# Kernel optimization log

Hardware: AMD Instinct MI355X
Metric: run time of the kernel (lower is better)

The kernel has to match this reference:

```python
import jax, jax.numpy as jnp
import numpy as np

QSIGN = jnp.array([1.0, -1.0, -1.0, -1.0], dtype=jnp.float32)
IDENT = jnp.array([1.0, 0.0, 0.0, 0.0], dtype=jnp.float32)


def quat_multiply(a, b):
    aw, ax, ay, az = a[..., 0], a[..., 1], a[..., 2], a[..., 3]
    bw, bx, by, bz = b[..., 0], b[..., 1], b[..., 2], b[..., 3]
    return jnp.stack([
        aw * bw - ax * bx - ay * by - az * bz,
        aw * bx + ax * bw + ay * bz - az * by,
        aw * by - ax * bz + ay * bw + az * bx,
        aw * bz + ax * by - ay * bx + az * bw], axis=-1)


def quat_to_rot(q):
    w, x, y, z = q[..., 0], q[..., 1], q[..., 2], q[..., 3]
    r = jnp.stack([
        w * w + x * x - y * y - z * z, 2 * (x * y - w * z), 2 * (x * z + w * y),
        2 * (x * y + w * z), w * w - x * x + y * y - z * z, 2 * (y * z - w * x),
        2 * (x * z - w * y), 2 * (y * z + w * x), w * w - x * x - y * y + z * z], axis=-1)
    return r.reshape(q.shape[:-1] + (3, 3))


def quat_rotate(q, v):
    return jnp.einsum('...ij,...j->...i', quat_to_rot(q), v)


def mlp(z, W1, b1, W2, b2):
    return jax.nn.relu(z @ W1 + b1) @ W2 + b2


def setup_inputs() -> dict:
    key = jax.random.key(0)
    ks = jax.random.split(key, 24)
    B, N, H, E, M, O, T = 2, 512, 64, 32, 64, 64, 64
    x = jax.random.normal(ks[0], (B, N, 3), dtype=jnp.float32)
    q = jax.random.normal(ks[1], (B, N, 4), dtype=jnp.float32)
    q = q / jnp.linalg.norm(q, axis=-1, keepdims=True)  # unit quats
    h = jax.random.normal(ks[2], (B, N, H), dtype=jnp.float32)
    e = jax.random.normal(ks[3], (B, N, N, E), dtype=jnp.float32)
    node_mask = jnp.ones((B, N), dtype=bool)

    def lin(k, fi, fo):
        return jax.random.normal(k, (fi, fo), dtype=jnp.float32) / np.sqrt(fi)

    msg_in = 2 * H + E + 9  # 169
    inp = dict(x=x, quats=q, h=h, e=e, node_mask=node_mask,
               Wm1=lin(ks[4], msg_in, T), bm1=jnp.zeros((T,)),
               Wm2=lin(ks[5], T, M), bm2=jnp.zeros((M,)),
               Wf1=lin(ks[6], H + M, T), bf1=jnp.zeros((T,)),
               Wf2=lin(ks[7], T, O), bf2=jnp.zeros((O,)),
               Wt1=lin(ks[8], M, T), bt1=jnp.zeros((T,)),
               Wt2=lin(ks[9], T, 3), bt2=jnp.zeros((3,)),
               Wq1=lin(ks[10], M, T), bq1=jnp.zeros((T,)),
               Wq2=lin(ks[11], T, 4), bq2=jnp.zeros((4,)))
    return inp


def reference(x, quats, h, e, node_mask,
              Wm1, bm1, Wm2, bm2, Wf1, bf1, Wf2, bf2,
              Wt1, bt1, Wt2, bt2, Wq1, bq1, Wq2, bq2):
    B, N, H = h.shape
    eye = jnp.eye(N, dtype=bool)[None]
    msg_mask = node_mask[:, :, None] & node_mask[:, None, :] & ~eye  # [B,N,N]
    n_nodes = node_mask.sum(axis=-1).astype(x.dtype)  # [B]

    # inverse frame of node j: rot = conj(q_j)/|q_j|^2, applied as R_j^-1 (x_i - t_j)
    q_inv = (quats * QSIGN) / jnp.sum(quats * quats, axis=-1, keepdims=True)

    diff = x[:, :, None, :] - x[:, None, :, :]            # [B,N,N,3], x_i - x_j
    d2 = jnp.sum(diff * diff, axis=-1)                    # [B,N,N]
    qdot = jnp.abs(jnp.einsum('bik,bjk->bij', quats, quats))
    local_x = quat_rotate(q_inv[:, None, :, :], diff)     # R_j^-1 (x_i - x_j)
    local_q = quat_multiply(q_inv[:, None, :, :], quats[:, :, None, :])  # q_j^-1 * q_i

    hi = jnp.broadcast_to(h[:, :, None, :], (B, N, N, H))
    hj = jnp.broadcast_to(h[:, None, :, :], (B, N, N, H))
    feat = jnp.concatenate([hi, hj, e, local_x, local_q,
                            d2[..., None], qdot[..., None]], axis=-1)

    m = mlp(feat, Wm1, bm1, Wm2, bm2) * msg_mask[..., None]  # [B,N,N,M]
    msum = m.sum(axis=-2)                                    # [B,N,M]

    o = mlp(jnp.concatenate([h, msum], axis=-1), Wf1, bf1, Wf2, bf2)

    dx = mlp(m, Wt1, bt1, Wt2, bt2) * msg_mask[..., None]    # [B,N,N,3]

    dq = mlp(msum, Wq1, bq1, Wq2, bq2)                       # [B,N,4]
    dq = jnp.where(node_mask[..., None], dq, IDENT)
    dq = dq / jnp.maximum(jnp.linalg.norm(dq, axis=-1, keepdims=True), 1e-12)

    upd_q = quat_multiply(quats, dq)
    upd_q = jnp.where(node_mask[..., None], upd_q, IDENT)
    upd_q = upd_q / jnp.linalg.norm(upd_q, axis=-1, keepdims=True)  # normalize_quats=True

    # rotate dx[i,j] by updated frame of node j, aggregate over j
    rot_dx = quat_rotate(upd_q[:, None, :, :], dx).sum(axis=-2)     # [B,N,3]
    upd_x = x + rot_dx / (n_nodes[:, None, None] - 1.0)
    return upd_q, upd_x, o
```

## Files before the change

### kernel.cpp

```cpp
#include <hip/hip_runtime.h>
#include <math.h>
#include <stdint.h>

#define B_ 2
#define N_ 512

#define WS_WBF   0
#define WS_NGEO  7680
#define WS_APRE  15872
#define WS_BPREF 81408
#define WS_MPART 146944
#define WS_DXBUF 278016

typedef short short8v __attribute__((ext_vector_type(8)));
typedef float f32x4 __attribute__((ext_vector_type(4)));

union FragU { int4 i; short8v s; };
union PackU { uint32_t w[4]; short8v s; };

static __device__ inline uint32_t pk2(float lo, float hi) {
    uint32_t r;
    asm volatile("v_cvt_pk_bf16_f32 %0, %1, %2" : "=v"(r) : "v"(lo), "v"(hi));
    return r;
}
static __device__ inline short f2bs(float f) {
    uint32_t u = __float_as_uint(f);
    u = (u + 0x7FFFu + ((u >> 16) & 1u)) >> 16;
    return (short)u;
}

__global__ void k_prep(const float* __restrict__ Wm1, const float* __restrict__ Wm2,
                       const float* __restrict__ Wt1, const float* __restrict__ Wt2,
                       short* __restrict__ wbf)
{
    const int id = blockIdx.x * 256 + threadIdx.x;
    if (id < 4608) {
        const int ch = id / 72, p = id % 72;
        float v1 = 0.f, v2 = 0.f, v3 = 0.f;
        if (p < 64) {
            if (p < 32) v1 = Wm1[(128 + p) * 64 + ch];
            else if (p < 41) v1 = Wm1[(160 + p - 32) * 64 + ch];
            const int s = p >> 5, ee = p & 7, gg = (p >> 3) & 3;
            const int k1 = 32 * s + 16 * (ee >> 2) + 4 * gg + (ee & 3);
            v2 = Wm2[k1 * 64 + ch];
            v3 = Wt1[k1 * 64 + ch];
        }
        wbf[id] = f2bs(v1);
        wbf[4608 + id] = f2bs(v2);
        wbf[9216 + id] = f2bs(v3);
    } else if (id < 5760) {
        const int idx = id - 4608;
        const int d = idx / 72, p = idx % 72;
        float v = 0.f;
        if (p < 64 && d < 3) {
            const int s = p >> 5, ee = p & 7, gg = (p >> 3) & 3;
            const int k1 = 32 * s + 16 * (ee >> 2) + 4 * gg + (ee & 3);
            v = Wt2[k1 * 3 + d];
        }
        wbf[13824 + idx] = f2bs(v);
    }
}

__global__ __launch_bounds__(256) void k_node_pre(
    const float* __restrict__ x,
    const float* __restrict__ quats,
    const float* __restrict__ h,
    const float* __restrict__ Wm1,
    const float* __restrict__ bm1,
    float* __restrict__ ngeo,
    float* __restrict__ Apre,
    float* __restrict__ BpreF)
{
    __shared__ float sW[128 * 64];
    __shared__ float sh[4][64];

    const int tid = threadIdx.x;
    for (int idx = tid; idx < 128 * 64 / 4; idx += 256)
        ((float4*)sW)[idx] = ((const float4*)Wm1)[idx];

    const int wv = tid >> 6;
    const int c = tid & 63;
    const int node = blockIdx.x * 4 + wv;

    sh[wv][c] = h[node * 64 + c];
    __syncthreads();

    float a = bm1[c];
    float bv = 0.f;
#pragma unroll 8
    for (int k = 0; k < 64; ++k) {
        const float hk = sh[wv][k];
        a  = fmaf(hk, sW[k * 64 + c], a);
        bv = fmaf(hk, sW[(64 + k) * 64 + c], bv);
    }
    Apre[node * 64 + c] = a;
    const int aa = c >> 4, gg = (c >> 2) & 3, bb = c & 3;
    BpreF[(node >> 4) * 1024 + ((node & 15) + 16 * gg) * 16 + 4 * aa + bb] = bv;

    if (c == 0) {
        ngeo[node * 8 + 0] = x[node * 3 + 0];
        ngeo[node * 8 + 1] = x[node * 3 + 1];
        ngeo[node * 8 + 2] = x[node * 3 + 2];
        ngeo[node * 8 + 3] = 0.f;
        ngeo[node * 8 + 4] = quats[node * 4 + 0];
        ngeo[node * 8 + 5] = quats[node * 4 + 1];
        ngeo[node * 8 + 6] = quats[node * 4 + 2];
        ngeo[node * 8 + 7] = quats[node * 4 + 3];
    }
}

__global__ __launch_bounds__(512, 2) void k_edge(
    const float* __restrict__ e,
    const float* __restrict__ ngeo,
    const float* __restrict__ Apre,
    const float* __restrict__ BpreF,
    const short* __restrict__ wbf,
    const float* __restrict__ bm2,
    const float* __restrict__ bt1,
    const float* __restrict__ bt2,
    float* __restrict__ mpart, float* __restrict__ dxbuf)
{
    __shared__ __align__(16) short Ws[14976];
    __shared__ float msLDS[4][64];

    const int tid = threadIdx.x;

    for (int idx = tid; idx < 1872; idx += 512)
        ((int4*)Ws)[idx] = ((const int4*)wbf)[idx];
    __syncthreads();

    const short* W1s = Ws;
    const short* W2s = Ws + 4608;
    const short* W3s = Ws + 9216;
    const short* W4s = Ws + 13824;

    const int w = tid >> 6;
    const int l = tid & 63;
    const int g = l >> 4;
    const int c = l & 15;

    const int ig = blockIdx.x >> 1;
    const int half = blockIdx.x & 1;
    const int ni = ig * 4 + (w >> 1);
    const int b = ni >> 9;
    const int i = ni & 511;
    const int quarter = half * 2 + (w & 1);
    const int j0w = quarter * 128;

    const float4 gi0 = ((const float4*)ngeo)[ni * 2 + 0];
    const float4 gi1 = ((const float4*)ngeo)[ni * 2 + 1];
    const float xi0 = gi0.x, xi1 = gi0.y, xi2 = gi0.z;
    const float qi0 = gi1.x, qi1 = gi1.y, qi2 = gi1.z, qi3 = gi1.w;

    float apre[16], bm2r[16], bt1r[16], bt2r[4];
#pragma unroll
    for (int q = 0; q < 16; ++q) {
        const int row = 16 * (q >> 2) + 4 * g + (q & 3);
        apre[q] = Apre[ni * 64 + row];
        bm2r[q] = bm2[row];
        bt1r[q] = bt1[row];
    }
#pragma unroll
    for (int q = 0; q < 4; ++q) {
        const int d = 4 * g + q;
        bt2r[q] = (d < 3) ? bt2[d] : 0.f;
    }

    float msum[16];
#pragma unroll
    for (int q = 0; q < 16; ++q) msum[q] = 0.f;

#pragma unroll 2
    for (int t = 0; t < 8; ++t) {
        const int j0m = j0w + t * 16;
        const int nj = b * N_ + j0m + c;

        const float* ep = e + ((size_t)(b * N_ + i) * N_ + j0m + c) * 32 + g * 8;
        const float4 e0 = *(const float4*)ep;
        const float4 e1 = *(const float4*)(ep + 4);
        const float4 n0 = ((const float4*)ngeo)[nj * 2 + 0];
        const float4 n1 = ((const float4*)ngeo)[nj * 2 + 1];
        const float* bp = BpreF + (size_t)(nj >> 4) * 1024 + l * 16;
        const float4 bi0 = ((const float4*)bp)[0];
        const float4 bi1 = ((const float4*)bp)[1];
        const float4 bi2 = ((const float4*)bp)[2];
        const float4 bi3 = ((const float4*)bp)[3];

        const float xj0 = n0.x, xj1 = n0.y, xj2 = n0.z;
        const float qj0 = n1.x, qj1 = n1.y, qj2 = n1.z, qj3 = n1.w;
        const float dsum = qj0 * qj0 + qj1 * qj1 + qj2 * qj2 + qj3 * qj3;
        const float inv = __builtin_amdgcn_rcpf(dsum);
        const float qw = qj0 * inv, qx = -qj1 * inv;
        const float qy = -qj2 * inv, qz = -qj3 * inv;
        const float d0 = xi0 - xj0, d1 = xi1 - xj1, d2v = xi2 - xj2;
        const float dd = d0 * d0 + d1 * d1 + d2v * d2v;
        const float qd = fabsf(qi0 * qj0 + qi1 * qj1 + qi2 * qj2 + qi3 * qj3);
        const float ww = qw * qw, xx = qx * qx, yy = qy * qy, zz = qz * qz;
        const float xy = qx * qy, xz = qx * qz, yz = qy * qz;
        const float wx = qw * qx, wy = qw * qy, wz = qw * qz;
        const float lx0 = (ww + xx - yy - zz) * d0 + 2.f * (xy - wz) * d1 + 2.f * (xz + wy) * d2v;
        const float lx1 = 2.f * (xy + wz) * d0 + (ww - xx + yy - zz) * d1 + 2.f * (yz - wx) * d2v;
        const float lx2 = 2.f * (xz - wy) * d0 + 2.f * (yz + wx) * d1 + (ww - xx - yy + zz) * d2v;
        const float lq0 = qw * qi0 - qx * qi1 - qy * qi2 - qz * qi3;
        const float lq1 = qw * qi1 + qx * qi0 + qy * qi3 - qz * qi2;
        const float lq2 = qw * qi2 - qx * qi3 + qy * qi0 + qz * qi1;
        const float lq3 = qw * qi3 + qx * qi2 - qy * qi1 + qz * qi0;

        PackU y0, yg;
        y0.w[0] = pk2(e0.x, e0.y); y0.w[1] = pk2(e0.z, e0.w);
        y0.w[2] = pk2(e1.x, e1.y); y0.w[3] = pk2(e1.z, e1.w);
        const uint32_t w0 = pk2(lx0, lx1), w1 = pk2(lx2, lq0);
        const uint32_t w2 = pk2(lq1, lq2), w3 = pk2(lq3, dd);
        const uint32_t wq = pk2(qd, 0.f);
        yg.w[0] = (g == 0) ? w0 : ((g == 1) ? wq : 0u);
        yg.w[1] = (g == 0) ? w1 : 0u;
        yg.w[2] = (g == 0) ? w2 : 0u;
        yg.w[3] = (g == 0) ? w3 : 0u;

        f32x4 acc1[4];
        acc1[0][0] = apre[0] + bi0.x;  acc1[0][1] = apre[1] + bi0.y;
        acc1[0][2] = apre[2] + bi0.z;  acc1[0][3] = apre[3] + bi0.w;
        acc1[1][0] = apre[4] + bi1.x;  acc1[1][1] = apre[5] + bi1.y;
        acc1[1][2] = apre[6] + bi1.z;  acc1[1][3] = apre[7] + bi1.w;
        acc1[2][0] = apre[8] + bi2.x;  acc1[2][1] = apre[9] + bi2.y;
        acc1[2][2] = apre[10] + bi2.z; acc1[2][3] = apre[11] + bi2.w;
        acc1[3][0] = apre[12] + bi3.x; acc1[3][1] = apre[13] + bi3.y;
        acc1[3][2] = apre[14] + bi3.z; acc1[3][3] = apre[15] + bi3.w;
#pragma unroll
        for (int nt = 0; nt < 4; ++nt) {
            FragU xw0, xw1;
            xw0.i = *(const int4*)&W1s[(16 * nt + c) * 72 + g * 8];
            xw1.i = *(const int4*)&W1s[(16 * nt + c) * 72 + 32 + g * 8];
            acc1[nt] = __builtin_amdgcn_mfma_f32_16x16x32_bf16(xw0.s, y0.s, acc1[nt], 0, 0, 0);
            acc1[nt] = __builtin_amdgcn_mfma_f32_16x16x32_bf16(xw1.s, yg.s, acc1[nt], 0, 0, 0);
        }

        PackU by1[2];
#pragma unroll
        for (int s = 0; s < 2; ++s) {
            const f32x4 a0 = acc1[2 * s], a1 = acc1[2 * s + 1];
            by1[s].w[0] = pk2(fmaxf(a0[0], 0.f), fmaxf(a0[1], 0.f));
            by1[s].w[1] = pk2(fmaxf(a0[2], 0.f), fmaxf(a0[3], 0.f));
            by1[s].w[2] = pk2(fmaxf(a1[0], 0.f), fmaxf(a1[1], 0.f));
            by1[s].w[3] = pk2(fmaxf(a1[2], 0.f), fmaxf(a1[3], 0.f));
        }

        f32x4 acc2[4];
#pragma unroll
        for (int nt = 0; nt < 4; ++nt) {
            acc2[nt][0] = bm2r[nt * 4 + 0]; acc2[nt][1] = bm2r[nt * 4 + 1];
            acc2[nt][2] = bm2r[nt * 4 + 2]; acc2[nt][3] = bm2r[nt * 4 + 3];
        }
#pragma unroll
        for (int nt = 0; nt < 4; ++nt)
#pragma unroll
            for (int s = 0; s < 2; ++s) {
                FragU xw;
                xw.i = *(const int4*)&W2s[(16 * nt + c) * 72 + s * 32 + g * 8];
                acc2[nt] = __builtin_amdgcn_mfma_f32_16x16x32_bf16(
                    xw.s, by1[s].s, acc2[nt], 0, 0, 0);
            }

        const float maskf = (j0m + c == i) ? 0.f : 1.f;
#pragma unroll
        for (int nt = 0; nt < 4; ++nt) {
            acc2[nt][0] *= maskf; acc2[nt][1] *= maskf;
            acc2[nt][2] *= maskf; acc2[nt][3] *= maskf;
            msum[nt * 4 + 0] += acc2[nt][0];
            msum[nt * 4 + 1] += acc2[nt][1];
            msum[nt * 4 + 2] += acc2[nt][2];
            msum[nt * 4 + 3] += acc2[nt][3];
        }

        PackU by2[2];
#pragma unroll
        for (int s = 0; s < 2; ++s) {
            const f32x4 a0 = acc2[2 * s], a1 = acc2[2 * s + 1];
            by2[s].w[0] = pk2(a0[0], a0[1]);
            by2[s].w[1] = pk2(a0[2], a0[3]);
            by2[s].w[2] = pk2(a1[0], a1[1]);
            by2[s].w[3] = pk2(a1[2], a1[3]);
        }

        f32x4 acc3[4];
#pragma unroll
        for (int nt = 0; nt < 4; ++nt) {
            acc3[nt][0] = bt1r[nt * 4 + 0]; acc3[nt][1] = bt1r[nt * 4 + 1];
            acc3[nt][2] = bt1r[nt * 4 + 2]; acc3[nt][3] = bt1r[nt * 4 + 3];
        }
#pragma unroll
        for (int nt = 0; nt < 4; ++nt)
#pragma unroll
            for (int s = 0; s < 2; ++s) {
                FragU xw;
                xw.i = *(const int4*)&W3s[(16 * nt + c) * 72 + s * 32 + g * 8];
                acc3[nt] = __builtin_amdgcn_mfma_f32_16x16x32_bf16(
                    xw.s, by2[s].s, acc3[nt], 0, 0, 0);
            }

        PackU by3[2];
#pragma unroll
        for (int s = 0; s < 2; ++s) {
            const f32x4 a0 = acc3[2 * s], a1 = acc3[2 * s + 1];
            by3[s].w[0] = pk2(fmaxf(a0[0], 0.f), fmaxf(a0[1], 0.f));
            by3[s].w[1] = pk2(fmaxf(a0[2], 0.f), fmaxf(a0[3], 0.f));
            by3[s].w[2] = pk2(fmaxf(a1[0], 0.f), fmaxf(a1[1], 0.f));
            by3[s].w[3] = pk2(fmaxf(a1[2], 0.f), fmaxf(a1[3], 0.f));
        }

        f32x4 acc4;
        acc4[0] = bt2r[0]; acc4[1] = bt2r[1]; acc4[2] = bt2r[2]; acc4[3] = bt2r[3];
#pragma unroll
        for (int s = 0; s < 2; ++s) {
            FragU xw;
            xw.i = *(const int4*)&W4s[c * 72 + s * 32 + g * 8];
            acc4 = __builtin_amdgcn_mfma_f32_16x16x32_bf16(
                xw.s, by3[s].s, acc4, 0, 0, 0);
        }
        if (g == 0) {
            float4 o4;
            o4.x = acc4[0] * maskf; o4.y = acc4[1] * maskf;
            o4.z = acc4[2] * maskf; o4.w = 0.f;
            ((float4*)dxbuf)[(size_t)ni * N_ + j0m + c] = o4;
        }
    }

#pragma unroll
    for (int q = 0; q < 16; ++q) {
        float v = msum[q];
        v += __shfl_xor(v, 1); v += __shfl_xor(v, 2);
        v += __shfl_xor(v, 4); v += __shfl_xor(v, 8);
        msum[q] = v;
    }
    __syncthreads();
    if ((w & 1) && c == 0) {
#pragma unroll
        for (int q = 0; q < 16; ++q)
            msLDS[w >> 1][16 * (q >> 2) + 4 * g + (q & 3)] = msum[q];
    }
    __syncthreads();
    if (!(w & 1) && c == 0) {
#pragma unroll
        for (int nt = 0; nt < 4; ++nt) {
            float4 mo;
            mo.x = msum[nt * 4 + 0] + msLDS[w >> 1][16 * nt + 4 * g + 0];
            mo.y = msum[nt * 4 + 1] + msLDS[w >> 1][16 * nt + 4 * g + 1];
            mo.z = msum[nt * 4 + 2] + msLDS[w >> 1][16 * nt + 4 * g + 2];
            mo.w = msum[nt * 4 + 3] + msLDS[w >> 1][16 * nt + 4 * g + 3];
            *(float4*)&mpart[((size_t)(half * (B_ * N_) + ni)) * 64 + 16 * nt + 4 * g] = mo;
        }
    }
}

__global__ __launch_bounds__(256) void k_node_post(
    const float* __restrict__ quats,
    const float* __restrict__ h,
    const float* __restrict__ mpart,
    const float* __restrict__ Wf1, const float* __restrict__ bf1,
    const float* __restrict__ Wf2, const float* __restrict__ bf2,
    const float* __restrict__ Wq1, const float* __restrict__ bq1,
    const float* __restrict__ Wq2, const float* __restrict__ bq2,
    float* __restrict__ out_q, float* __restrict__ out_o)
{
    __shared__ float sWf1[128 * 64];
    __shared__ float sWf2[64 * 64];
    __shared__ float sWq1[64 * 64];
    __shared__ float sWq2[64 * 4];
    __shared__ float sh[4][64], sm[4][64], stf[4][64], stq[4][64];

    const int tid = threadIdx.x;
    for (int idx = tid; idx < 128 * 64 / 4; idx += 256)
        ((float4*)sWf1)[idx] = ((const float4*)Wf1)[idx];
    for (int idx = tid; idx < 64 * 64 / 4; idx += 256) {
        ((float4*)sWf2)[idx] = ((const float4*)Wf2)[idx];
        ((float4*)sWq1)[idx] = ((const float4*)Wq1)[idx];
    }
    if (tid < 64) {
        sWq2[tid * 4 + 0] = Wq2[tid * 4 + 0];
        sWq2[tid * 4 + 1] = Wq2[tid * 4 + 1];
        sWq2[tid * 4 + 2] = Wq2[tid * 4 + 2];
        sWq2[tid * 4 + 3] = Wq2[tid * 4 + 3];
    }

    const int wv = tid >> 6;
    const int c = tid & 63;
    const int node = blockIdx.x * 4 + wv;

    const float ms = mpart[(size_t)node * 64 + c] +
                     mpart[((size_t)(B_ * N_) + node) * 64 + c];
    sm[wv][c] = ms;
    sh[wv][c] = h[node * 64 + c];
    __syncthreads();

    float accf = bf1[c];
    float accq = bq1[c];
#pragma unroll 8
    for (int k = 0; k < 64; ++k) {
        const float hk = sh[wv][k];
        const float mk = sm[wv][k];
        accf = fmaf(hk, sWf1[k * 64 + c], accf);
        accf = fmaf(mk, sWf1[(64 + k) * 64 + c], accf);
        accq = fmaf(mk, sWq1[k * 64 + c], accq);
    }
    stf[wv][c] = fmaxf(accf, 0.f);
    stq[wv][c] = fmaxf(accq, 0.f);
    __syncthreads();

    float o = bf2[c];
#pragma unroll 8
    for (int k = 0; k < 64; ++k) o = fmaf(stf[wv][k], sWf2[k * 64 + c], o);
    out_o[(size_t)node * 64 + c] = o;

    {
        const int d = c & 3, kb = c >> 2;
        float p = 0.f;
#pragma unroll
        for (int m = 0; m < 4; ++m) {
            const int kk = kb + 16 * m;
            p = fmaf(stq[wv][kk], sWq2[kk * 4 + d], p);
        }
        p += __shfl_xor(p, 4);  p += __shfl_xor(p, 8);
        p += __shfl_xor(p, 16); p += __shfl_xor(p, 32);
        const float p0 = __shfl(p, 0), p1 = __shfl(p, 1);
        const float p2 = __shfl(p, 2), p3 = __shfl(p, 3);
        if (c == 0) {
            float dq0 = p0 + bq2[0], dq1 = p1 + bq2[1];
            float dq2 = p2 + bq2[2], dq3 = p3 + bq2[3];
            const float nrm = sqrtf(dq0 * dq0 + dq1 * dq1 + dq2 * dq2 + dq3 * dq3);
            const float inv = 1.f / fmaxf(nrm, 1e-12f);
            const float b0 = dq0 * inv, b1 = dq1 * inv, b2 = dq2 * inv, b3 = dq3 * inv;
            const float aw = quats[node * 4 + 0], ax = quats[node * 4 + 1];
            const float ay = quats[node * 4 + 2], az = quats[node * 4 + 3];
            float u0 = aw * b0 - ax * b1 - ay * b2 - az * b3;
            float u1 = aw * b1 + ax * b0 + ay * b3 - az * b2;
            float u2 = aw * b2 - ax * b3 + ay * b0 + az * b1;
            float u3 = aw * b3 + ax * b2 - ay * b1 + az * b0;
            const float n2 = sqrtf(u0 * u0 + u1 * u1 + u2 * u2 + u3 * u3);
            u0 /= n2; u1 /= n2; u2 /= n2; u3 /= n2;
            out_q[node * 4 + 0] = u0; out_q[node * 4 + 1] = u1;
            out_q[node * 4 + 2] = u2; out_q[node * 4 + 3] = u3;
        }
    }
}

__global__ void k_aggregate(const float* __restrict__ x,
                            const float* __restrict__ out_q,
                            const float* __restrict__ dxbuf,
                            float* __restrict__ out_x)
{
    const int node = blockIdx.x;
    const int b = node >> 9;
    const int tid = threadIdx.x;

    float s0 = 0.f, s1 = 0.f, s2 = 0.f;
    for (int j = tid; j < N_; j += 256) {
        const float4 d4 = ((const float4*)dxbuf)[(size_t)node * N_ + j];
        const float4 q4 = ((const float4*)out_q)[b * N_ + j];
        const float w = q4.x, X = q4.y, Y = q4.z, Z = q4.w;
        const float ww = w * w, xx = X * X, yy = Y * Y, zz = Z * Z;
        const float xy = X * Y, xz = X * Z, yz = Y * Z;
        const float wx = w * X, wy = w * Y, wz = w * Z;
        s0 += (ww + xx - yy - zz) * d4.x + 2.f * (xy - wz) * d4.y + 2.f * (xz + wy) * d4.z;
        s1 += 2.f * (xy + wz) * d4.x + (ww - xx + yy - zz) * d4.y + 2.f * (yz - wx) * d4.z;
        s2 += 2.f * (xz - wy) * d4.x + 2.f * (yz + wx) * d4.y + (ww - xx - yy + zz) * d4.z;
    }
#pragma unroll
    for (int off = 1; off <= 32; off <<= 1) {
        s0 += __shfl_xor(s0, off);
        s1 += __shfl_xor(s1, off);
        s2 += __shfl_xor(s2, off);
    }
    __shared__ float red[4][3];
    const int wave = tid >> 6, lane = tid & 63;
    if (lane == 0) { red[wave][0] = s0; red[wave][1] = s1; red[wave][2] = s2; }
    __syncthreads();
    if (tid == 0) {
        const float t0 = red[0][0] + red[1][0] + red[2][0] + red[3][0];
        const float t1 = red[0][1] + red[1][1] + red[2][1] + red[3][1];
        const float t2 = red[0][2] + red[1][2] + red[2][2] + red[3][2];
        const float inv = 1.f / (float)(N_ - 1);
        out_x[node * 3 + 0] = x[node * 3 + 0] + t0 * inv;
        out_x[node * 3 + 1] = x[node * 3 + 1] + t1 * inv;
        out_x[node * 3 + 2] = x[node * 3 + 2] + t2 * inv;
    }
}

extern "C" void kernel_launch(void* const* d_in, const int* in_sizes, int n_in,
                              void* d_out, int out_size, void* d_ws, size_t ws_size,
                              hipStream_t stream) {
    const float* x     = (const float*)d_in[0];
    const float* quats = (const float*)d_in[1];
    const float* h     = (const float*)d_in[2];
    const float* e     = (const float*)d_in[3];
    const float* Wm1 = (const float*)d_in[5];
    const float* bm1 = (const float*)d_in[6];
    const float* Wm2 = (const float*)d_in[7];
    const float* bm2 = (const float*)d_in[8];
    const float* Wf1 = (const float*)d_in[9];
    const float* bf1 = (const float*)d_in[10];
    const float* Wf2 = (const float*)d_in[11];
    const float* bf2 = (const float*)d_in[12];
    const float* Wt1 = (const float*)d_in[13];
    const float* bt1 = (const float*)d_in[14];
    const float* Wt2 = (const float*)d_in[15];
    const float* bt2 = (const float*)d_in[16];
    const float* Wq1 = (const float*)d_in[17];
    const float* bq1 = (const float*)d_in[18];
    const float* Wq2 = (const float*)d_in[19];
    const float* bq2 = (const float*)d_in[20];

    float* out = (float*)d_out;
    float* out_q = out;
    float* out_x = out + 4096;
    float* out_o = out + 7168;

    float* ws    = (float*)d_ws;
    short* wbf   = (short*)(ws + WS_WBF);
    float* ngeo  = ws + WS_NGEO;
    float* Apre  = ws + WS_APRE;
    float* BpreF = ws + WS_BPREF;
    float* mpart = ws + WS_MPART;
    float* dxbuf = ws + WS_DXBUF;

    k_prep<<<dim3(23), dim3(256), 0, stream>>>(Wm1, Wm2, Wt1, Wt2, wbf);

    k_node_pre<<<dim3(B_ * N_ / 4), dim3(256), 0, stream>>>(
        x, quats, h, Wm1, bm1, ngeo, Apre, BpreF);

    k_edge<<<dim3(512), dim3(512), 0, stream>>>(
        e, ngeo, Apre, BpreF, wbf, bm2, bt1, bt2, mpart, dxbuf);

    k_node_post<<<dim3(B_ * N_ / 4), dim3(256), 0, stream>>>(
        quats, h, mpart, Wf1, bf1, Wf2, bf2, Wq1, bq1, Wq2, bq2,
        out_q, out_o);

    k_aggregate<<<dim3(B_ * N_), dim3(256), 0, stream>>>(
        x, out_q, dxbuf, out_x);
}
```

Before: 175.3 us.

## Fuse weight prep into node_pre and remap edge kernel to one node per block

Folds the bf16 weight-packing kernel into k_node_pre, removing one launch. The edge kernel now runs 1024 blocks of 256 threads, one node per block with four waves each covering 128 neighbours, under launch bounds of (256,5) instead of (512,2). Biases move from per-thread registers into shared memory, which cuts register pressure so more waves can be resident. The per-node message sum is now reduced fully inside the block, so node_post reads one partial instead of two, in exchange for an extra LDS reduction step.

```diff
diff --git a/kernel.cpp b/kernel.cpp
--- a/kernel.cpp
+++ b/kernel.cpp
@@ -10,7 +10,7 @@
 #define WS_APRE  15872
 #define WS_BPREF 81408
 #define WS_MPART 146944
-#define WS_DXBUF 278016
+#define WS_DXBUF 212480
 
 typedef short short8v __attribute__((ext_vector_type(8)));
 typedef float f32x4 __attribute__((ext_vector_type(4)));
@@ -27,38 +27,6 @@
     uint32_t u = __float_as_uint(f);
     u = (u + 0x7FFFu + ((u >> 16) & 1u)) >> 16;
     return (short)u;
-}
-
-__global__ void k_prep(const float* __restrict__ Wm1, const float* __restrict__ Wm2,
-                       const float* __restrict__ Wt1, const float* __restrict__ Wt2,
-                       short* __restrict__ wbf)
-{
-    const int id = blockIdx.x * 256 + threadIdx.x;
-    if (id < 4608) {
-        const int ch = id / 72, p = id % 72;
-        float v1 = 0.f, v2 = 0.f, v3 = 0.f;
-        if (p < 64) {
-            if (p < 32) v1 = Wm1[(128 + p) * 64 + ch];
-            else if (p < 41) v1 = Wm1[(160 + p - 32) * 64 + ch];
-            const int s = p >> 5, ee = p & 7, gg = (p >> 3) & 3;
-            const int k1 = 32 * s + 16 * (ee >> 2) + 4 * gg + (ee & 3);
-            v2 = Wm2[k1 * 64 + ch];
-            v3 = Wt1[k1 * 64 + ch];
-        }
-        wbf[id] = f2bs(v1);
-        wbf[4608 + id] = f2bs(v2);
-        wbf[9216 + id] = f2bs(v3);
-    } else if (id < 5760) {
-        const int idx = id - 4608;
-        const int d = idx / 72, p = idx % 72;
-        float v = 0.f;
-        if (p < 64 && d < 3) {
-            const int s = p >> 5, ee = p & 7, gg = (p >> 3) & 3;
-            const int k1 = 32 * s + 16 * (ee >> 2) + 4 * gg + (ee & 3);
-            v = Wt2[k1 * 3 + d];
-        }
-        wbf[13824 + idx] = f2bs(v);
-    }
 }
 
 __global__ __launch_bounds__(256) void k_node_pre(
@@ -67,6 +35,10 @@
     const float* __restrict__ h,
     const float* __restrict__ Wm1,
     const float* __restrict__ bm1,
+    const float* __restrict__ Wm2,
+    const float* __restrict__ Wt1,
+    const float* __restrict__ Wt2,
+    short* __restrict__ wbf,
     float* __restrict__ ngeo,
     float* __restrict__ Apre,
     float* __restrict__ BpreF)
@@ -75,6 +47,36 @@
     __shared__ float sh[4][64];
 
     const int tid = threadIdx.x;
+
+    {
+        const int id = blockIdx.x * 256 + tid;
+        if (id < 4608) {
+            const int ch = id / 72, p = id % 72;
+            float v1 = 0.f, v2 = 0.f, v3 = 0.f;
+            if (p < 64) {
+                if (p < 32) v1 = Wm1[(128 + p) * 64 + ch];
+                else if (p < 41) v1 = Wm1[(160 + p - 32) * 64 + ch];
+                const int s = p >> 5, ee = p & 7, gg = (p >> 3) & 3;
+                const int k1 = 32 * s + 16 * (ee >> 2) + 4 * gg + (ee & 3);
+                v2 = Wm2[k1 * 64 + ch];
+                v3 = Wt1[k1 * 64 + ch];
+            }
+            wbf[id] = f2bs(v1);
+            wbf[4608 + id] = f2bs(v2);
+            wbf[9216 + id] = f2bs(v3);
+        } else if (id < 5760) {
+            const int idx = id - 4608;
+            const int d = idx / 72, p = idx % 72;
+            float v = 0.f;
+            if (p < 64 && d < 3) {
+                const int s = p >> 5, ee = p & 7, gg = (p >> 3) & 3;
+                const int k1 = 32 * s + 16 * (ee >> 2) + 4 * gg + (ee & 3);
+                v = Wt2[k1 * 3 + d];
+            }
+            wbf[13824 + idx] = f2bs(v);
+        }
+    }
+
     for (int idx = tid; idx < 128 * 64 / 4; idx += 256)
         ((float4*)sW)[idx] = ((const float4*)Wm1)[idx];
 
@@ -109,7 +111,7 @@
     }
 }
 
-__global__ __launch_bounds__(512, 2) void k_edge(
+__global__ __launch_bounds__(256, 5) void k_edge(
     const float* __restrict__ e,
     const float* __restrict__ ngeo,
     const float* __restrict__ Apre,
@@ -121,12 +123,15 @@
     float* __restrict__ mpart, float* __restrict__ dxbuf)
 {
     __shared__ __align__(16) short Ws[14976];
-    __shared__ float msLDS[4][64];
+    __shared__ __align__(16) float sbias[132];
+    __shared__ float msLDS[3][64];
 
     const int tid = threadIdx.x;
 
-    for (int idx = tid; idx < 1872; idx += 512)
+    for (int idx = tid; idx < 1872; idx += 256)
         ((int4*)Ws)[idx] = ((const int4*)wbf)[idx];
+    if (tid < 64) { sbias[tid] = bm2[tid]; sbias[64 + tid] = bt1[tid]; }
+    if (tid >= 64 && tid < 68) sbias[128 + (tid - 64)] = (tid - 64 < 3) ? bt2[tid - 64] : 0.f;
     __syncthreads();
 
     const short* W1s = Ws;
@@ -139,32 +144,26 @@
     const int g = l >> 4;
     const int c = l & 15;
 
-    const int ig = blockIdx.x >> 1;
-    const int half = blockIdx.x & 1;
-    const int ni = ig * 4 + (w >> 1);
+    const int ni = blockIdx.x;
     const int b = ni >> 9;
     const int i = ni & 511;
-    const int quarter = half * 2 + (w & 1);
-    const int j0w = quarter * 128;
+    const int j0w = w * 128;
 
     const float4 gi0 = ((const float4*)ngeo)[ni * 2 + 0];
     const float4 gi1 = ((const float4*)ngeo)[ni * 2 + 1];
     const float xi0 = gi0.x, xi1 = gi0.y, xi2 = gi0.z;
     const float qi0 = gi1.x, qi1 = gi1.y, qi2 = gi1.z, qi3 = gi1.w;
 
-    float apre[16], bm2r[16], bt1r[16], bt2r[4];
+    float apre[16], bt2r[4];
 #pragma unroll
     for (int q = 0; q < 16; ++q) {
         const int row = 16 * (q >> 2) + 4 * g + (q & 3);
         apre[q] = Apre[ni * 64 + row];
-        bm2r[q] = bm2[row];
-        bt1r[q] = bt1[row];
-    }
-#pragma unroll
-    for (int q = 0; q < 4; ++q) {
-        const int d = 4 * g + q;
-        bt2r[q] = (d < 3) ? bt2[d] : 0.f;
-    }
+    }
+#pragma unroll
+    for (int q = 0; q < 4; ++q) bt2r[q] = sbias[128 + ((4 * g + q < 3) ? 4 * g + q : 3)];
+#pragma unroll
+    for (int q = 0; q < 4; ++q) if (4 * g + q >= 3) bt2r[q] = 0.f;
 
     float msum[16];
 #pragma unroll
@@ -247,10 +246,8 @@
 
         f32x4 acc2[4];
 #pragma unroll
-        for (int nt = 0; nt < 4; ++nt) {
-            acc2[nt][0] = bm2r[nt * 4 + 0]; acc2[nt][1] = bm2r[nt * 4 + 1];
-            acc2[nt][2] = bm2r[nt * 4 + 2]; acc2[nt][3] = bm2r[nt * 4 + 3];
-        }
+        for (int nt = 0; nt < 4; ++nt)
+            acc2[nt] = *(const f32x4*)&sbias[16 * nt + 4 * g];
 #pragma unroll
         for (int nt = 0; nt < 4; ++nt)
 #pragma unroll
@@ -284,10 +281,8 @@
 
         f32x4 acc3[4];
 #pragma unroll
-        for (int nt = 0; nt < 4; ++nt) {
-            acc3[nt][0] = bt1r[nt * 4 + 0]; acc3[nt][1] = bt1r[nt * 4 + 1];
-            acc3[nt][2] = bt1r[nt * 4 + 2]; acc3[nt][3] = bt1r[nt * 4 + 3];
-        }
+        for (int nt = 0; nt < 4; ++nt)
+            acc3[nt] = *(const f32x4*)&sbias[64 + 16 * nt + 4 * g];
 #pragma unroll
         for (int nt = 0; nt < 4; ++nt)
 #pragma unroll
@@ -333,21 +328,25 @@
         msum[q] = v;
     }
     __syncthreads();
-    if ((w & 1) && c == 0) {
+    if (w > 0 && c == 0) {
 #pragma unroll
         for (int q = 0; q < 16; ++q)
-            msLDS[w >> 1][16 * (q >> 2) + 4 * g + (q & 3)] = msum[q];
-    }
-    __syncthreads();
-    if (!(w & 1) && c == 0) {
+            msLDS[w - 1][16 * (q >> 2) + 4 * g + (q & 3)] = msum[q];
+    }
+    __syncthreads();
+    if (w == 0 && c == 0) {
 #pragma unroll
         for (int nt = 0; nt < 4; ++nt) {
             float4 mo;
-            mo.x = msum[nt * 4 + 0] + msLDS[w >> 1][16 * nt + 4 * g + 0];
-            mo.y = msum[nt * 4 + 1] + msLDS[w >> 1][16 * nt + 4 * g + 1];
-            mo.z = msum[nt * 4 + 2] + msLDS[w >> 1][16 * nt + 4 * g + 2];
-            mo.w = msum[nt * 4 + 3] + msLDS[w >> 1][16 * nt + 4 * g + 3];
-            *(float4*)&mpart[((size_t)(half * (B_ * N_) + ni)) * 64 + 16 * nt + 4 * g] = mo;
+            mo.x = msum[nt * 4 + 0] + msLDS[0][16 * nt + 4 * g + 0]
+                 + msLDS[1][16 * nt + 4 * g + 0] + msLDS[2][16 * nt + 4 * g + 0];
+            mo.y = msum[nt * 4 + 1] + msLDS[0][16 * nt + 4 * g + 1]
+                 + msLDS[1][16 * nt + 4 * g + 1] + msLDS[2][16 * nt + 4 * g + 1];
+            mo.z = msum[nt * 4 + 2] + msLDS[0][16 * nt + 4 * g + 2]
+                 + msLDS[1][16 * nt + 4 * g + 2] + msLDS[2][16 * nt + 4 * g + 2];
+            mo.w = msum[nt * 4 + 3] + msLDS[0][16 * nt + 4 * g + 3]
+                 + msLDS[1][16 * nt + 4 * g + 3] + msLDS[2][16 * nt + 4 * g + 3];
+            *(float4*)&mpart[(size_t)ni * 64 + 16 * nt + 4 * g] = mo;
         }
     }
 }
@@ -386,8 +385,7 @@
     const int c = tid & 63;
     const int node = blockIdx.x * 4 + wv;
 
-    const float ms = mpart[(size_t)node * 64 + c] +
-                     mpart[((size_t)(B_ * N_) + node) * 64 + c];
+    const float ms = mpart[(size_t)node * 64 + c];
     sm[wv][c] = ms;
     sh[wv][c] = h[node * 64 + c];
     __syncthreads();
@@ -522,12 +520,10 @@
     float* mpart = ws + WS_MPART;
     float* dxbuf = ws + WS_DXBUF;
 
-    k_prep<<<dim3(23), dim3(256), 0, stream>>>(Wm1, Wm2, Wt1, Wt2, wbf);
-
     k_node_pre<<<dim3(B_ * N_ / 4), dim3(256), 0, stream>>>(
-        x, quats, h, Wm1, bm1, ngeo, Apre, BpreF);
-
-    k_edge<<<dim3(512), dim3(512), 0, stream>>>(
+        x, quats, h, Wm1, bm1, Wm2, Wt1, Wt2, wbf, ngeo, Apre, BpreF);
+
+    k_edge<<<dim3(1024), dim3(256), 0, stream>>>(
         e, ngeo, Apre, BpreF, wbf, bm2, bt1, bt2, mpart, dxbuf);
 
     k_node_post<<<dim3(B_ * N_ / 4), dim3(256), 0, stream>>>(
```

Measured after the change: 225.3 us. 1.28x slower.
